# Kernel optimization log

Hardware: AMD Instinct MI355X
Metric: run time of the kernel (lower is better)

The kernel has to match this reference:

```python
import jax, jax.numpy as jnp
import numpy as np

NUM_GRAPHS = 16


def gat_layer(x, src, dst, n, W, a_s, a_d, b):
    # PyG GATConv, concat=False (mean over heads), negative_slope=0.2
    H, C = a_s.shape
    h = (x @ W).reshape(x.shape[0], H, C)            # [N,H,C]
    es = jnp.einsum('nhc,hc->nh', h, a_s)            # alpha_src per node
    ed = jnp.einsum('nhc,hc->nh', h, a_d)            # alpha_dst per node
    e = jax.nn.leaky_relu(es[src] + ed[dst], 0.2)    # [E,H]
    m = jax.ops.segment_max(e, dst, num_segments=n)
    m = jnp.where(jnp.isfinite(m), m, 0.0)
    p = jnp.exp(e - m[dst])
    denom = jax.ops.segment_sum(p, dst, num_segments=n)
    alpha = p / (denom[dst] + 1e-16)                 # segment softmax over in-edges
    out = jax.ops.segment_sum(h[src] * alpha[..., None], dst, num_segments=n)  # [N,H,C]
    return out.mean(axis=1) + b


def _forward(x, edge_index, batch,
             W_e0, a_s_e0, a_d_e0, b_e0, W_e1, a_s_e1, a_d_e1, b_e1,
             W_d0, a_s_d0, a_d_d0, b_d0, W_d1, a_s_d1, a_d_d1, b_d1,
             g_w1, g_b1, g_w2, g_b2):
    n = x.shape[0]
    loop = jnp.arange(n, dtype=edge_index.dtype)     # PyG add_self_loops=True
    src = jnp.concatenate([edge_index[0], loop])
    dst = jnp.concatenate([edge_index[1], loop])
    # encoder (dropout inert in eval)
    h = jax.nn.relu(gat_layer(x, src, dst, n, W_e0, a_s_e0, a_d_e0, b_e0))
    h = gat_layer(h, src, dst, n, W_e1, a_s_e1, a_d_e1, b_e1)
    # GlobalAttention pooling: gate MLP -> segment softmax over graphs -> scatter sum
    gate = (jax.nn.relu(h @ g_w1 + g_b1) @ g_w2 + g_b2)[:, 0]   # [N]
    gm = jax.ops.segment_max(gate, batch, num_segments=NUM_GRAPHS)
    gm = jnp.where(jnp.isfinite(gm), gm, 0.0)
    p = jnp.exp(gate - gm[batch])
    att = p / (jax.ops.segment_sum(p, batch, num_segments=NUM_GRAPHS)[batch] + 1e-16)
    pooled = jax.ops.segment_sum(att[:, None] * h, batch, num_segments=NUM_GRAPHS)
    h = pooled[batch]                                # broadcast pooled back to nodes
    # decoder (heads=1)
    h = jax.nn.relu(gat_layer(h, src, dst, n, W_d0, a_s_d0, a_d_d0, b_d0))
    return gat_layer(h, src, dst, n, W_d1, a_s_d1, a_d_d1, b_d1)


def setup_inputs() -> dict:
    key = jax.random.key(0)
    ks = jax.random.split(key, 24)
    N, E, Din, H, C = 50000, 250000, 128, 8, 64
    def w(k, shape, fan_in):
        return (jax.random.normal(k, shape, jnp.float32) / np.sqrt(fan_in)).astype(jnp.float32)
    return {
        'x': jax.random.normal(ks[0], (N, Din), jnp.float32),
        'edge_index': jax.random.randint(ks[1], (2, E), 0, N, dtype=jnp.int32),
        'batch': jnp.sort(jax.random.randint(ks[2], (N,), 0, NUM_GRAPHS, dtype=jnp.int32)),
        'W_e0': w(ks[3], (Din, H * C), Din), 'a_s_e0': w(ks[4], (H, C), C), 'a_d_e0': w(ks[5], (H, C), C), 'b_e0': w(ks[6], (C,), C),
        'W_e1': w(ks[7], (C, H * C), C), 'a_s_e1': w(ks[8], (H, C), C), 'a_d_e1': w(ks[9], (H, C), C), 'b_e1': w(ks[10], (C,), C),
        'W_d0': w(ks[11], (C, C), C), 'a_s_d0': w(ks[12], (1, C), C), 'a_d_d0': w(ks[13], (1, C), C), 'b_d0': w(ks[14], (C,), C),
        'W_d1': w(ks[15], (C, Din), C), 'a_s_d1': w(ks[16], (1, Din), Din), 'a_d_d1': w(ks[17], (1, Din), Din), 'b_d1': w(ks[18], (Din,), Din),
        'g_w1': w(ks[19], (C, C), C), 'g_b1': w(ks[20], (C,), C), 'g_w2': w(ks[21], (C, 1), C), 'g_b2': w(ks[22], (1,), C),
    }


def reference(x, edge_index, batch,
              W_e0, a_s_e0, a_d_e0, b_e0, W_e1, a_s_e1, a_d_e1, b_e1,
              W_d0, a_s_d0, a_d_d0, b_d0, W_d1, a_s_d1, a_d_d1, b_d1,
              g_w1, g_b1, g_w2, g_b2):
    return _forward(x, edge_index, batch,
                    W_e0, a_s_e0, a_d_e0, b_e0, W_e1, a_s_e1, a_d_e1, b_e1,
                    W_d0, a_s_d0, a_d_d0, b_d0, W_d1, a_s_d1, a_d_d1, b_d1,
                    g_w1, g_b1, g_w2, g_b2)
```

## Files before the change

kernel.cpp:

```cpp
#include <hip/hip_runtime.h>
#include <hip/hip_fp16.h>
#include <math.h>

#define TB 256

typedef _Float16 half8v __attribute__((ext_vector_type(8)));
typedef float float4v __attribute__((ext_vector_type(4)));

static __device__ __forceinline__ int edge_src(const int* ei, int E, int e) {
    return (e < E) ? ei[e] : (e - E);
}
static __device__ __forceinline__ int edge_dst(const int* ei, int E, int e) {
    return (e < E) ? ei[E + e] : (e - E);
}

__global__ void csr_count(const int* __restrict__ ei, int E, int Etot, int* __restrict__ cnt) {
    int e = blockIdx.x * blockDim.x + threadIdx.x;
    if (e >= Etot) return;
    atomicAdd(&cnt[edge_dst(ei, E, e)], 1);
}

__global__ __launch_bounds__(256) void scan_phase1(const int* __restrict__ cnt,
                                                   int* __restrict__ incl,
                                                   int* __restrict__ bsum, int n) {
    __shared__ int sdata[256];
    int t = threadIdx.x;
    int base = blockIdx.x * 256;
    int v = (base + t < n) ? cnt[base + t] : 0;
    for (int d = 1; d < 256; d <<= 1) {
        sdata[t] = v; __syncthreads();
        if (t >= d) v += sdata[t - d];
        __syncthreads();
    }
    if (base + t < n) incl[base + t] = v;
    if (t == 255) bsum[blockIdx.x] = v;
}

__global__ void scan_phase2(int* bsum, int nb) {
    __shared__ int sdata[256];
    int t = threadIdx.x;
    int v = (t < nb) ? bsum[t] : 0;
    for (int d = 1; d < 256; d <<= 1) {
        sdata[t] = v; __syncthreads();
        if (t >= d) v += sdata[t - d];
        __syncthreads();
    }
    if (t < nb) bsum[t] = v;
}

__global__ __launch_bounds__(256) void scan_phase3(const int* __restrict__ incl,
                                                   const int* __restrict__ bsum,
                                                   int* __restrict__ off, int n) {
    int i = blockIdx.x * 256 + threadIdx.x;
    if (i < n) off[i + 1] = incl[i] + (blockIdx.x ? bsum[blockIdx.x - 1] : 0);
    if (i == 0) off[0] = 0;
}

__global__ void csr_fill(const int* __restrict__ ei, int E, int Etot,
                         const int* __restrict__ off, int* __restrict__ cur,
                         int* __restrict__ esrc) {
    int e = blockIdx.x * blockDim.x + threadIdx.x;
    if (e >= Etot) return;
    int d = edge_dst(ei, E, e);
    int pos = atomicAdd(&cur[d], 1);
    esrc[off[d] + pos] = edge_src(ei, E, e);
}

__global__ void find_gstart(const int* __restrict__ batch, int* __restrict__ gstart, int N) {
    int n = blockIdx.x * blockDim.x + threadIdx.x;
    if (n >= N) return;
    int b = batch[n];
    int prev = n ? batch[n - 1] : -1;
    for (int g = prev + 1; g <= b; ++g) gstart[g] = n;
    if (n == N - 1)
        for (int g = b + 1; g <= 16; ++g) gstart[g] = N;
}

__global__ void cast_f2h(const float* __restrict__ in, __half* __restrict__ out, int n) {
    int i2 = (blockIdx.x * blockDim.x + threadIdx.x) * 2;
    if (i2 + 1 < n) {
        float2 v = *(const float2*)(in + i2);
        *(__half2*)(out + i2) = __floats2half2_rn(v.x, v.y);
    } else if (i2 < n) {
        out[i2] = __float2half(in[i2]);
    }
}

__global__ void make_ws(const float* __restrict__ W, const float* __restrict__ a_s,
                        const float* __restrict__ a_d, float* __restrict__ ws,
                        float* __restrict__ wd, int K, int H, int C) {
    int i = blockIdx.x * blockDim.x + threadIdx.x;
    if (i >= H * K) return;
    int h = i / K, k = i % K;
    const float* wrow = W + (size_t)k * H * C + h * C;
    float s = 0.f, d = 0.f;
    for (int c = 0; c < C; ++c) {
        s += wrow[c] * a_s[h * C + c];
        d += wrow[c] * a_d[h * C + c];
    }
    ws[i] = s;
    wd[i] = d;
}

__global__ void transpose_cast(const float* __restrict__ W, __half* __restrict__ WT,
                               int K, int N) {
    int i = blockIdx.x * blockDim.x + threadIdx.x;
    if (i >= N * K) return;
    int nn = i / K, kk = i % K;
    WT[i] = __float2half(W[kk * N + nn]);
}

__global__ void make_wstackT(const float* __restrict__ W, __half* __restrict__ WT,
                             int K, int H, int C) {
    int i = blockIdx.x * blockDim.x + threadIdx.x;
    if (i >= K * H * C) return;
    int c = i / (H * K);
    int rem = i % (H * K);
    int h = rem / K, k = rem % K;
    WT[i] = __float2half(W[(size_t)k * H * C + h * C + c]);
}

template <int K>
__global__ __launch_bounds__(256) void gemm_mfma(const __half* __restrict__ A,
                                                 const __half* __restrict__ BT,
                                                 __half* __restrict__ C,
                                                 int M, int N) {
    constexpr int KP = K + 8;
    __shared__ __align__(16) __half As[64 * KP];
    __shared__ __align__(16) __half Bs[64 * KP];
    int tid = threadIdx.x;
    int bm = blockIdx.y * 64, bn = blockIdx.x * 64;
    constexpr int LPR = K / 8;
    for (int idx = tid; idx < 64 * LPR; idx += 256) {
        int row = idx / LPR, koff = (idx % LPR) * 8;
        uint4 v = make_uint4(0u, 0u, 0u, 0u);
        int gr = bm + row;
        if (gr < M) v = *(const uint4*)(A + (size_t)gr * K + koff);
        *(uint4*)(&As[row * KP + koff]) = v;
        uint4 wv = *(const uint4*)(BT + (size_t)(bn + row) * K + koff);
        *(uint4*)(&Bs[row * KP + koff]) = wv;
    }
    __syncthreads();
    int wv_ = tid >> 6, l = tid & 63;
    int lr = l & 15, g = l >> 4;
    float4v acc[4] = {{0.f, 0.f, 0.f, 0.f}, {0.f, 0.f, 0.f, 0.f},
                      {0.f, 0.f, 0.f, 0.f}, {0.f, 0.f, 0.f, 0.f}};
    const __half* ap = &As[(16 * wv_ + lr) * KP + 8 * g];
    const __half* bp = &Bs[lr * KP + 8 * g];
#pragma unroll
    for (int k0 = 0; k0 < K; k0 += 32) {
        half8v af = *reinterpret_cast<const half8v*>(ap + k0);
#pragma unroll
        for (int nt = 0; nt < 4; ++nt) {
            half8v bf = *reinterpret_cast<const half8v*>(bp + nt * 16 * KP + k0);
            acc[nt] = __builtin_amdgcn_mfma_f32_16x16x32_f16(af, bf, acc[nt], 0, 0, 0);
        }
    }
#pragma unroll
    for (int nt = 0; nt < 4; ++nt) {
#pragma unroll
        for (int r = 0; r < 4; ++r) {
            int grow = bm + 16 * wv_ + 4 * g + r;
            if (grow < M)
                C[(size_t)grow * N + bn + nt * 16 + lr] = __float2half(acc[nt][r]);
        }
    }
}

template <int K, int H>
__global__ __launch_bounds__(256) void scores_nt(const __half* __restrict__ A,
                                                 const float* __restrict__ ws,
                                                 const float* __restrict__ wd,
                                                 float* __restrict__ es,
                                                 float* __restrict__ ed, int N) {
    int n = blockIdx.x * blockDim.x + threadIdx.x;
    if (n >= N) return;
    const __half* row = A + (size_t)n * K;
    float s[H] = {}, d[H] = {};
#pragma unroll
    for (int k0 = 0; k0 < K; k0 += 8) {
        uint4 raw = *(const uint4*)(row + k0);
        const __half* hv = (const __half*)&raw;
        float a[8];
#pragma unroll
        for (int q = 0; q < 8; ++q) a[q] = __half2float(hv[q]);
#pragma unroll
        for (int h = 0; h < H; ++h)
#pragma unroll
            for (int q = 0; q < 8; ++q) {
                s[h] += a[q] * ws[h * K + k0 + q];
                d[h] += a[q] * wd[h * K + k0 + q];
            }
    }
#pragma unroll
    for (int h = 0; h < H; ++h) {
        es[(size_t)n * H + h] = s[h];
        ed[(size_t)n * H + h] = d[h];
    }
}

template <bool RELU>
__global__ __launch_bounds__(256) void gat_gather_h8(const __half* __restrict__ hsrc,
                                                     const float* __restrict__ es,
                                                     const float* __restrict__ ed,
                                                     const int* __restrict__ off,
                                                     const int* __restrict__ esrc,
                                                     const float* __restrict__ bias,
                                                     __half* __restrict__ out, int N) {
    constexpr int HC = 512;
    int n = (blockIdx.x * blockDim.x + threadIdx.x) >> 6;
    int lane = threadIdx.x & 63;
    if (n >= N) return;
    int hd = lane >> 3;
    int k8 = lane >> 3, h8 = lane & 7;
    int j0 = off[n], j1 = off[n + 1];

    float edl = ed[(size_t)n * 8 + h8];

    float acc[8] = {};
    float denacc = 0.f;
    for (int j = j0; j < j1; j += 8) {
        int jj = j + k8;
        int jc = (jj < j1) ? jj : (j1 - 1);
        int sidx = esrc[jc];
        float v = es[(size_t)sidx * 8 + h8] + edl;
        v = (v > 0.f) ? v : 0.2f * v;
        float pm = (jj < j1) ? expf(v) : 0.f;
        denacc += pm;
        uint4 rw[8];
#pragma unroll
        for (int k = 0; k < 8; ++k) {
            int sb = __shfl(sidx, k * 8);
            rw[k] = *(const uint4*)(hsrc + (size_t)sb * HC + 8 * lane);
        }
#pragma unroll
        for (int k = 0; k < 8; ++k) {
            float a = __shfl(pm, k * 8 + hd);
            const __half* hv = (const __half*)&rw[k];
#pragma unroll
            for (int q = 0; q < 8; ++q) acc[q] += a * __half2float(hv[q]);
        }
    }

    float den = denacc;
#pragma unroll
    for (int o = 8; o < 64; o <<= 1) den += __shfl_xor(den, o);
    float dv = __shfl(den, hd) + 1e-16f;

#pragma unroll
    for (int q = 0; q < 8; ++q) acc[q] /= dv;
#pragma unroll
    for (int o = 8; o < 64; o <<= 1)
#pragma unroll
        for (int q = 0; q < 8; ++q) acc[q] += __shfl_xor(acc[q], o);

    if (lane < 8) {
        int cbase = 8 * lane;
        float r[8];
#pragma unroll
        for (int q = 0; q < 8; ++q) {
            float o2 = acc[q] * 0.125f + bias[cbase + q];
            if (RELU) o2 = fmaxf(o2, 0.f);
            r[q] = o2;
        }
        __half2 p0 = __floats2half2_rn(r[0], r[1]);
        __half2 p1 = __floats2half2_rn(r[2], r[3]);
        __half2 p2 = __floats2half2_rn(r[4], r[5]);
        __half2 p3 = __floats2half2_rn(r[6], r[7]);
        uint4 pk;
        pk.x = *(unsigned*)&p0; pk.y = *(unsigned*)&p1;
        pk.z = *(unsigned*)&p2; pk.w = *(unsigned*)&p3;
        *(uint4*)(out + (size_t)n * 64 + cbase) = pk;
    }
}

__global__ __launch_bounds__(256) void gat_gather_zh8(const __half* __restrict__ A,
                                                      const float* __restrict__ es,
                                                      const float* __restrict__ ed,
                                                      const int* __restrict__ off,
                                                      const int* __restrict__ esrc,
                                                      __half* __restrict__ z, int N) {
    int n = (blockIdx.x * blockDim.x + threadIdx.x) >> 6;
    int lane = threadIdx.x & 63;
    if (n >= N) return;
    int h = lane >> 3, q = lane & 7;
    int j0 = off[n], j1 = off[n + 1];
    float edv = ed[(size_t)n * 8 + h];

    float acc[8] = {};
    float den = 0.f;
    int j = j0;
    for (; j + 1 < j1; j += 2) {
        int s0 = esrc[j], s1 = esrc[j + 1];
        float v0 = es[(size_t)s0 * 8 + h] + edv;
        float v1 = es[(size_t)s1 * 8 + h] + edv;
        v0 = (v0 > 0.f) ? v0 : 0.2f * v0;
        v1 = (v1 > 0.f) ? v1 : 0.2f * v1;
        float p0 = expf(v0), p1 = expf(v1);
        den += p0 + p1;
        uint4 r0 = *(const uint4*)(A + (size_t)s0 * 64 + 8 * q);
        uint4 r1 = *(const uint4*)(A + (size_t)s1 * 64 + 8 * q);
        const __half* h0 = (const __half*)&r0;
        const __half* h1 = (const __half*)&r1;
#pragma unroll
        for (int k = 0; k < 8; ++k)
            acc[k] += p0 * __half2float(h0[k]) + p1 * __half2float(h1[k]);
    }
    if (j < j1) {
        int s0 = esrc[j];
        float v0 = es[(size_t)s0 * 8 + h] + edv;
        v0 = (v0 > 0.f) ? v0 : 0.2f * v0;
        float p0 = expf(v0);
        den += p0;
        uint4 r0 = *(const uint4*)(A + (size_t)s0 * 64 + 8 * q);
        const __half* h0 = (const __half*)&r0;
#pragma unroll
        for (int k = 0; k < 8; ++k) acc[k] += p0 * __half2float(h0[k]);
    }

    float inv = 1.f / ((den + 1e-16f) * 8.f);
    float r[8];
#pragma unroll
    for (int k = 0; k < 8; ++k) r[k] = acc[k] * inv;
    __half2 p0 = __floats2half2_rn(r[0], r[1]);
    __half2 p1 = __floats2half2_rn(r[2], r[3]);
    __half2 p2 = __floats2half2_rn(r[4], r[5]);
    __half2 p3 = __floats2half2_rn(r[6], r[7]);
    uint4 pk;
    pk.x = *(unsigned*)&p0; pk.y = *(unsigned*)&p1;
    pk.z = *(unsigned*)&p2; pk.w = *(unsigned*)&p3;
    *(uint4*)(z + (size_t)n * 512 + h * 64 + 8 * q) = pk;
}

__global__ __launch_bounds__(256) void gat_gather_z8(const __half* __restrict__ A,
                                                     const float* __restrict__ es,
                                                     const float* __restrict__ ed,
                                                     const int* __restrict__ off,
                                                     const int* __restrict__ esrc,
                                                     __half* __restrict__ z, int N) {
    int n = (blockIdx.x * blockDim.x + threadIdx.x) >> 6;
    int lane = threadIdx.x & 63;
    if (n >= N) return;
    int k8 = lane >> 3, q8 = lane & 7;
    int j0 = off[n], j1 = off[n + 1];
    float edv = ed[n];

    float acc[8] = {};
    float denacc = 0.f;
    for (int j = j0; j < j1; j += 8) {
        int jj = j + k8;
        int jc = (jj < j1) ? jj : (j1 - 1);
        int sidx = esrc[jc];
        float v = es[sidx] + edv;
        v = (v > 0.f) ? v : 0.2f * v;
        float pm = (jj < j1) ? expf(v) : 0.f;
        denacc += pm;
        uint4 rw = *(const uint4*)(A + (size_t)sidx * 64 + 8 * q8);
        const __half* hv = (const __half*)&rw;
#pragma unroll
        for (int q = 0; q < 8; ++q) acc[q] += pm * __half2float(hv[q]);
    }

    float den = denacc;
#pragma unroll
    for (int o = 8; o < 64; o <<= 1) {
        den += __shfl_xor(den, o);
#pragma unroll
        for (int q = 0; q < 8; ++q) acc[q] += __shfl_xor(acc[q], o);
    }
    float inv = 1.f / (den + 1e-16f);
    if (lane < 8) {
        float r[8];
#pragma unroll
        for (int q = 0; q < 8; ++q) r[q] = acc[q] * inv;
        __half2 p0 = __floats2half2_rn(r[0], r[1]);
        __half2 p1 = __floats2half2_rn(r[2], r[3]);
        __half2 p2 = __floats2half2_rn(r[4], r[5]);
        __half2 p3 = __floats2half2_rn(r[6], r[7]);
        uint4 pk;
        pk.x = *(unsigned*)&p0; pk.y = *(unsigned*)&p1;
        pk.z = *(unsigned*)&p2; pk.w = *(unsigned*)&p3;
        *(uint4*)(z + (size_t)n * 64 + 8 * lane) = pk;
    }
}

template <int KK, typename OUTT, bool RELU>
__global__ __launch_bounds__(256) void gemm_kt(const __half* __restrict__ A,
                                               const __half* __restrict__ BT,
                                               const float* __restrict__ bias,
                                               OUTT* __restrict__ C,
                                               int M, int Nout) {
    __shared__ __align__(16) __half As[64 * 72];
    __shared__ __align__(16) __half Bs[64 * 72];
    int tid = threadIdx.x;
    int bm = blockIdx.y * 64, bn = blockIdx.x * 64;
    int wv = tid >> 6, l = tid & 63, lr = l & 15, g = l >> 4;
    float4v acc[4] = {{0.f, 0.f, 0.f, 0.f}, {0.f, 0.f, 0.f, 0.f},
                      {0.f, 0.f, 0.f, 0.f}, {0.f, 0.f, 0.f, 0.f}};
    for (int kc = 0; kc < KK; kc += 64) {
        __syncthreads();
        for (int idx = tid; idx < 512; idx += 256) {
            int row = idx >> 3, ko = (idx & 7) * 8;
            uint4 v = make_uint4(0u, 0u, 0u, 0u);
            int gr = bm + row;
            if (gr < M) v = *(const uint4*)(A + (size_t)gr * KK + kc + ko);
            *(uint4*)(&As[row * 72 + ko]) = v;
            uint4 wvv = *(const uint4*)(BT + (size_t)(bn + row) * KK + kc + ko);
            *(uint4*)(&Bs[row * 72 + ko]) = wvv;
        }
        __syncthreads();
#pragma unroll
        for (int k0 = 0; k0 < 64; k0 += 32) {
            half8v af = *reinterpret_cast<const half8v*>(&As[(16 * wv + lr) * 72 + k0 + 8 * g]);
#pragma unroll
            for (int nt = 0; nt < 4; ++nt) {
                half8v bf = *reinterpret_cast<const half8v*>(&Bs[(nt * 16 + lr) * 72 + k0 + 8 * g]);
                acc[nt] = __builtin_amdgcn_mfma_f32_16x16x32_f16(af, bf, acc[nt], 0, 0, 0);
            }
        }
    }
#pragma unroll
    for (int nt = 0; nt < 4; ++nt) {
        float b = bias[bn + nt * 16 + lr];
#pragma unroll
        for (int r = 0; r < 4; ++r) {
            int grow = bm + 16 * wv + 4 * g + r;
            if (grow < M) {
                float c = acc[nt][r] + b;
                if (RELU) c = fmaxf(c, 0.f);
                if constexpr (sizeof(OUTT) == 2)
                    C[(size_t)grow * Nout + bn + nt * 16 + lr] = __float2half(c);
                else
                    C[(size_t)grow * Nout + bn + nt * 16 + lr] = c;
            }
        }
    }
}

__global__ __launch_bounds__(256) void gat_gather_d08(const float* __restrict__ hsrc,
                                                      const float* __restrict__ es16,
                                                      const float* __restrict__ ed16,
                                                      const int* __restrict__ off,
                                                      const int* __restrict__ esrc,
                                                      const int* __restrict__ batch,
                                                      const float* __restrict__ bias,
                                                      __half* __restrict__ out, int N) {
    int n = (blockIdx.x * blockDim.x + threadIdx.x) >> 6;
    int lane = threadIdx.x & 63;
    if (n >= N) return;
    int k8 = lane >> 3, q8 = lane & 7;
    int j0 = off[n], j1 = off[n + 1];
    float edv = ed16[batch[n]];

    float acc[8] = {};
    float denacc = 0.f;
    for (int j = j0; j < j1; j += 8) {
        int jj = j + k8;
        int jc = (jj < j1) ? jj : (j1 - 1);
        int g = batch[esrc[jc]];
        float v = es16[g] + edv;
        v = (v > 0.f) ? v : 0.2f * v;
        float pm = (jj < j1) ? expf(v) : 0.f;
        denacc += pm;
        const float* row = hsrc + (size_t)g * 64 + 8 * q8;
        float4 r0 = *(const float4*)row;
        float4 r1 = *(const float4*)(row + 4);
        acc[0] += pm * r0.x; acc[1] += pm * r0.y;
        acc[2] += pm * r0.z; acc[3] += pm * r0.w;
        acc[4] += pm * r1.x; acc[5] += pm * r1.y;
        acc[6] += pm * r1.z; acc[7] += pm * r1.w;
    }

    float den = denacc;
#pragma unroll
    for (int o = 8; o < 64; o <<= 1) {
        den += __shfl_xor(den, o);
#pragma unroll
        for (int q = 0; q < 8; ++q) acc[q] += __shfl_xor(acc[q], o);
    }
    float inv = 1.f / (den + 1e-16f);
    if (lane < 8) {
        float r[8];
#pragma unroll
        for (int q = 0; q < 8; ++q) r[q] = fmaxf(acc[q] * inv + bias[8 * lane + q], 0.f);
        __half2 p0 = __floats2half2_rn(r[0], r[1]);
        __half2 p1 = __floats2half2_rn(r[2], r[3]);
        __half2 p2 = __floats2half2_rn(r[4], r[5]);
        __half2 p3 = __floats2half2_rn(r[6], r[7]);
        uint4 pk;
        pk.x = *(unsigned*)&p0; pk.y = *(unsigned*)&p1;
        pk.z = *(unsigned*)&p2; pk.w = *(unsigned*)&p3;
        *(uint4*)(out + (size_t)n * 64 + 8 * lane) = pk;
    }
}

__global__ __launch_bounds__(256) void gate_mfma(const __half* __restrict__ A,
                                                 const __half* __restrict__ BT,
                                                 const float* __restrict__ b1,
                                                 const float* __restrict__ w2,
                                                 const float* __restrict__ b2,
                                                 const int* __restrict__ batch,
                                                 float* __restrict__ pg,
                                                 float* __restrict__ gden, int M) {
    constexpr int KP = 72;
    __shared__ __align__(16) __half As[64 * KP];
    __shared__ __align__(16) __half Bs[64 * KP];
    __shared__ float part[16];
    int tid = threadIdx.x;
    if (tid < 16) part[tid] = 0.f;
    int bm = blockIdx.x * 64;
    for (int idx = tid; idx < 512; idx += 256) {
        int row = idx >> 3, ko = (idx & 7) * 8;
        uint4 v = make_uint4(0u, 0u, 0u, 0u);
        int gr = bm + row;
        if (gr < M) v = *(const uint4*)(A + (size_t)gr * 64 + ko);
        *(uint4*)(&As[row * KP + ko]) = v;
        uint4 wvv = *(const uint4*)(BT + (size_t)row * 64 + ko);
        *(uint4*)(&Bs[row * KP + ko]) = wvv;
    }
    __syncthreads();
    int wv_ = tid >> 6, l = tid & 63;
    int lr = l & 15, g = l >> 4;
    float4v acc[4] = {{0.f, 0.f, 0.f, 0.f}, {0.f, 0.f, 0.f, 0.f},
                      {0.f, 0.f, 0.f, 0.f}, {0.f, 0.f, 0.f, 0.f}};
    const __half* ap = &As[(16 * wv_ + lr) * KP + 8 * g];
    const __half* bp = &Bs[lr * KP + 8 * g];
#pragma unroll
    for (int k0 = 0; k0 < 64; k0 += 32) {
        half8v af = *reinterpret_cast<const half8v*>(ap + k0);
#pragma unroll
        for (int nt = 0; nt < 4; ++nt) {
            half8v bf = *reinterpret_cast<const half8v*>(bp + nt * 16 * KP + k0);
            acc[nt] = __builtin_amdgcn_mfma_f32_16x16x32_f16(af, bf, acc[nt], 0, 0, 0);
        }
    }
    float partial[4];
#pragma unroll
    for (int r = 0; r < 4; ++r) {
        float t = 0.f;
#pragma unroll
        for (int nt = 0; nt < 4; ++nt) {
            int col = nt * 16 + lr;
            float tv = acc[nt][r] + b1[col];
            tv = fmaxf(tv, 0.f);
            t += tv * w2[col];
        }
        partial[r] = t;
    }
#pragma unroll
    for (int o = 1; o < 16; o <<= 1)
#pragma unroll
        for (int r = 0; r < 4; ++r) partial[r] += __shfl_xor(partial[r], o);
    if (lr == 0) {
        float bb = b2[0];
#pragma unroll
        for (int r = 0; r < 4; ++r) {
            int grow = bm + 16 * wv_ + 4 * g + r;
            if (grow < M) {
                float p = expf(partial[r] + bb);
                pg[grow] = p;
                atomicAdd(&part[batch[grow]], p);
            }
        }
    }
    __syncthreads();
    if (tid < 16 && part[tid] != 0.f) atomicAdd(&gden[tid], part[tid]);
}

#define POOL_SPLIT 32
__global__ __launch_bounds__(256) void pool_sum2(const __half* __restrict__ h,
                                                 const float* __restrict__ pg,
                                                 const int* __restrict__ gstart,
                                                 float* __restrict__ pooled, int N) {
    __shared__ float part[256];
    int g = blockIdx.x;
    int r0 = gstart[g], r1 = gstart[g + 1];
    int len = r1 - r0;
    int chunk = (len + POOL_SPLIT - 1) / POOL_SPLIT;
    int s0 = r0 + blockIdx.y * chunk;
    int s1 = min(s0 + chunk, r1);
    int wv = threadIdx.x >> 6, lane = threadIdx.x & 63;
    float acc = 0.f;
    for (int n = s0 + wv; n < s1; n += 4)
        acc += pg[n] * __half2float(h[(size_t)n * 64 + lane]);
    part[threadIdx.x] = acc;
    __syncthreads();
    if (threadIdx.x < 64) {
        float tot = part[threadIdx.x] + part[64 + threadIdx.x] +
                    part[128 + threadIdx.x] + part[192 + threadIdx.x];
        if (tot != 0.f) atomicAdd(&pooled[g * 64 + threadIdx.x], tot);
    }
}

__global__ void dec_prep(const float* __restrict__ pooled, const float* __restrict__ gden,
                         const float* __restrict__ Wd0, const float* __restrict__ asd,
                         const float* __restrict__ add, float* __restrict__ hd016,
                         float* __restrict__ es16, float* __restrict__ ed16) {
    int g = blockIdx.x;
    int lane = threadIdx.x;
    float pn = pooled[g * 64 + lane] / (gden[g] + 1e-16f);
    float o = 0.f;
    for (int c = 0; c < 64; ++c) o += __shfl(pn, c) * Wd0[c * 64 + lane];
    hd016[g * 64 + lane] = o;
    float s = o * asd[lane], d = o * add[lane];
#pragma unroll
    for (int off = 32; off; off >>= 1) {
        s += __shfl_xor(s, off);
        d += __shfl_xor(d, off);
    }
    if (lane == 0) {
        es16[g] = s;
        ed16[g] = d;
    }
}

static inline int cdiv(int a, int b) { return (a + b - 1) / b; }

extern "C" void kernel_launch(void* const* d_in, const int* in_sizes, int n_in,
                              void* d_out, int out_size, void* d_ws, size_t ws_size,
                              hipStream_t stream) {
    const float* x      = (const float*)d_in[0];
    const int*   ei     = (const int*)  d_in[1];
    const int*   batch  = (const int*)  d_in[2];
    const float* W_e0   = (const float*)d_in[3];
    const float* a_s_e0 = (const float*)d_in[4];
    const float* a_d_e0 = (const float*)d_in[5];
    const float* b_e0   = (const float*)d_in[6];
    const float* W_e1   = (const float*)d_in[7];
    const float* a_s_e1 = (const float*)d_in[8];
    const float* a_d_e1 = (const float*)d_in[9];
    const float* b_e1   = (const float*)d_in[10];
    const float* W_d0   = (const float*)d_in[11];
    const float* a_s_d0 = (const float*)d_in[12];
    const float* a_d_d0 = (const float*)d_in[13];
    const float* b_d0   = (const float*)d_in[14];
    const float* W_d1   = (const float*)d_in[15];
    const float* a_s_d1 = (const float*)d_in[16];
    const float* a_d_d1 = (const float*)d_in[17];
    const float* b_d1   = (const float*)d_in[18];
    const float* g_w1   = (const float*)d_in[19];
    const float* g_b1   = (const float*)d_in[20];
    const float* g_w2   = (const float*)d_in[21];
    const float* g_b2   = (const float*)d_in[22];

    const int N    = in_sizes[2];
    const int E    = in_sizes[1] / 2;
    const int Etot = E + N;
    const int Din  = in_sizes[0] / N;

    char* w = (char*)d_ws;
    size_t o = 0;
    auto alloc = [&](size_t bytes) -> void* {
        void* p = w + o;
        o = (o + bytes + 255) & ~(size_t)255;
        return p;
    };
    __half*   h16    = (__half*)  alloc((size_t)N * 512 * 2);
    __half*   x16    = (__half*)  alloc((size_t)N * Din * 2);
    __half*   bufA   = (__half*)  alloc((size_t)N * 64 * 2);
    __half*   bufB   = (__half*)  alloc((size_t)N * 64 * 2);
    __half*   wt_e0  = (__half*)  alloc((size_t)512 * 128 * 2);
    __half*   wst_e1 = (__half*)  alloc((size_t)64 * 512 * 2);
    __half*   wst_d1 = (__half*)  alloc((size_t)128 * 64 * 2);
    __half*   wt_g1  = (__half*)  alloc((size_t)64 * 64 * 2);
    float*    ws_e0  = (float*)   alloc(8 * 128 * 4);
    float*    wd_e0  = (float*)   alloc(8 * 128 * 4);
    float*    ws_e1  = (float*)   alloc(8 * 64 * 4);
    float*    wd_e1  = (float*)   alloc(8 * 64 * 4);
    float*    ws_d1  = (float*)   alloc(64 * 4);
    float*    wd_d1  = (float*)   alloc(64 * 4);
    float*    es     = (float*)   alloc((size_t)N * 8 * 4);
    float*    ed     = (float*)   alloc((size_t)N * 8 * 4);
    float*    pg     = (float*)   alloc((size_t)N * 4);
    int*      off    = (int*)     alloc((size_t)(N + 1) * 4);
    int*      cnt    = (int*)     alloc((size_t)N * 4);
    int*      esrc   = (int*)     alloc((size_t)Etot * 4);
    int*      bsum   = (int*)     alloc(256 * 4);
    int*      gstart = (int*)     alloc(17 * 4);
    float*    gden   = (float*)   alloc(16 * 4);
    float*    pooled = (float*)   alloc(16 * 64 * 4);
    float*    hd016  = (float*)   alloc(16 * 64 * 4);
    float*    es16   = (float*)   alloc(16 * 4);
    float*    ed16   = (float*)   alloc(16 * 4);
    (void)ws_size; (void)n_in; (void)out_size;

    const int nodeWaveGrid = cdiv(N, 4);
    const int nodeThreadGrid = cdiv(N, TB);
    const int edgeGrid     = cdiv(Etot, TB);
    const int scanBlocks   = cdiv(N, 256);

    hipMemsetAsync(cnt, 0, (size_t)N * 4, stream);
    csr_count<<<edgeGrid, TB, 0, stream>>>(ei, E, Etot, cnt);
    scan_phase1<<<scanBlocks, 256, 0, stream>>>(cnt, esrc , bsum, N);
    scan_phase2<<<1, 256, 0, stream>>>(bsum, scanBlocks);
    scan_phase3<<<scanBlocks, 256, 0, stream>>>(esrc, bsum, off, N);
    hipMemsetAsync(cnt, 0, (size_t)N * 4, stream);
    csr_fill<<<edgeGrid, TB, 0, stream>>>(ei, E, Etot, off, cnt, esrc);
    find_gstart<<<nodeThreadGrid, TB, 0, stream>>>(batch, gstart, N);

    cast_f2h<<<cdiv(N * Din / 2, TB), TB, 0, stream>>>(x, x16, N * Din);
    transpose_cast<<<cdiv(512 * 128, TB), TB, 0, stream>>>(W_e0, wt_e0, Din, 512);
    transpose_cast<<<cdiv(64 * 64, TB), TB, 0, stream>>>(g_w1, wt_g1, 64, 64);
    make_wstackT<<<cdiv(64 * 512, TB), TB, 0, stream>>>(W_e1, wst_e1, 64, 8, 64);
    make_wstackT<<<cdiv(128 * 64, TB), TB, 0, stream>>>(W_d1, wst_d1, 64, 1, 128);
    make_ws<<<cdiv(8 * 128, TB), TB, 0, stream>>>(W_e0, a_s_e0, a_d_e0, ws_e0, wd_e0, 128, 8, 64);
    make_ws<<<cdiv(8 * 64, TB), TB, 0, stream>>>(W_e1, a_s_e1, a_d_e1, ws_e1, wd_e1, 64, 8, 64);
    make_ws<<<1, TB, 0, stream>>>(W_d1, a_s_d1, a_d_d1, ws_d1, wd_d1, 64, 1, 128);

    scores_nt<128, 8><<<nodeThreadGrid, TB, 0, stream>>>(x16, ws_e0, wd_e0, es, ed, N);
    {
        dim3 grid(512 / 64, cdiv(N, 64));
        gemm_mfma<128><<<grid, TB, 0, stream>>>(x16, wt_e0, h16, N, 512);
    }
    gat_gather_h8<true><<<nodeWaveGrid, TB, 0, stream>>>(
        h16, es, ed, off, esrc, b_e0, bufA, N);

    scores_nt<64, 8><<<nodeThreadGrid, TB, 0, stream>>>(bufA, ws_e1, wd_e1, es, ed, N);
    gat_gather_zh8<<<nodeWaveGrid, TB, 0, stream>>>(bufA, es, ed, off, esrc, h16 , N);
    {
        dim3 grid(1, cdiv(N, 64));
        gemm_kt<512, __half, false><<<grid, TB, 0, stream>>>(h16 , wst_e1, b_e1, bufB, N, 64);
    }

    hipMemsetAsync(gden, 0, 16 * 4, stream);
    hipMemsetAsync(pooled, 0, 16 * 64 * 4, stream);
    gate_mfma<<<cdiv(N, 64), TB, 0, stream>>>(bufB, wt_g1, g_b1, g_w2, g_b2, batch, pg, gden, N);
    {
        dim3 grid(16, POOL_SPLIT);
        pool_sum2<<<grid, TB, 0, stream>>>(bufB, pg, gstart, pooled, N);
    }
    dec_prep<<<16, 64, 0, stream>>>(pooled, gden, W_d0, a_s_d0, a_d_d0, hd016, es16, ed16);

    gat_gather_d08<<<nodeWaveGrid, TB, 0, stream>>>(
        hd016, es16, ed16, off, esrc, batch, b_d0, bufA, N);

    scores_nt<64, 1><<<nodeThreadGrid, TB, 0, stream>>>(bufA, ws_d1, wd_d1, es, ed, N);
    gat_gather_z8<<<nodeWaveGrid, TB, 0, stream>>>(bufA, es, ed, off, esrc, h16 , N);
    {
        dim3 grid(2, cdiv(N, 64));
        gemm_kt<64, float, false><<<grid, TB, 0, stream>>>(h16 , wst_d1, b_d1, (float*)d_out, N, 128);
    }
}
```

Measured before the change: 352.6 us.

## Fuse weight prep kernels, fuse x cast into scores, widen first GEMM tile

The separate weight transpose/cast kernels and the three make_ws launches are merged into two launches. The fp32-to-fp16 cast of x is folded into the per-node score kernel, so x is read once instead of being cast and then reread. The first-layer GEMM now computes a 64x128 tile per block instead of 64x64, which halves how often A is reloaded but uses more LDS and accumulator registers per block. The combined score and cast kernel has each thread read a full fp32 row, which may coalesce poorly.

```diff
diff --git a/kernel.cpp b/kernel.cpp
--- a/kernel.cpp
+++ b/kernel.cpp
@@ -76,94 +76,142 @@
         for (int g = b + 1; g <= 16; ++g) gstart[g] = N;
 }
 
-__global__ void cast_f2h(const float* __restrict__ in, __half* __restrict__ out, int n) {
-    int i2 = (blockIdx.x * blockDim.x + threadIdx.x) * 2;
-    if (i2 + 1 < n) {
-        float2 v = *(const float2*)(in + i2);
-        *(__half2*)(out + i2) = __floats2half2_rn(v.x, v.y);
-    } else if (i2 < n) {
-        out[i2] = __float2half(in[i2]);
-    }
-}
-
-__global__ void make_ws(const float* __restrict__ W, const float* __restrict__ a_s,
-                        const float* __restrict__ a_d, float* __restrict__ ws,
-                        float* __restrict__ wd, int K, int H, int C) {
+__global__ void prep_weights(const float* __restrict__ W_e0, const float* __restrict__ g_w1,
+                             const float* __restrict__ W_e1, const float* __restrict__ W_d1,
+                             __half* __restrict__ wt_e0, __half* __restrict__ wt_g1,
+                             __half* __restrict__ wst_e1, __half* __restrict__ wst_d1) {
     int i = blockIdx.x * blockDim.x + threadIdx.x;
-    if (i >= H * K) return;
-    int h = i / K, k = i % K;
+    if (i < 65536) {
+        int nn = i / 128, kk = i % 128;
+        wt_e0[i] = __float2half(W_e0[kk * 512 + nn]);
+    } else if (i < 69632) {
+        int j = i - 65536;
+        int nn = j / 64, kk = j % 64;
+        wt_g1[j] = __float2half(g_w1[kk * 64 + nn]);
+    } else if (i < 102400) {
+        int j = i - 69632;
+        int c = j / 512, rem = j % 512;
+        int h = rem / 64, k = rem % 64;
+        wst_e1[j] = __float2half(W_e1[(size_t)k * 512 + h * 64 + c]);
+    } else if (i < 110592) {
+        int j = i - 102400;
+        int c = j / 64, k = j % 64;
+        wst_d1[j] = __float2half(W_d1[(size_t)k * 128 + c]);
+    }
+}
+
+__global__ void prep_ws(const float* __restrict__ W_e0, const float* __restrict__ a_s_e0,
+                        const float* __restrict__ a_d_e0,
+                        const float* __restrict__ W_e1, const float* __restrict__ a_s_e1,
+                        const float* __restrict__ a_d_e1,
+                        const float* __restrict__ W_d1, const float* __restrict__ a_s_d1,
+                        const float* __restrict__ a_d_d1,
+                        float* __restrict__ ws_e0, float* __restrict__ wd_e0,
+                        float* __restrict__ ws_e1, float* __restrict__ wd_e1,
+                        float* __restrict__ ws_d1, float* __restrict__ wd_d1) {
+    int i = blockIdx.x * blockDim.x + threadIdx.x;
+    const float* W; const float* as_; const float* ad_;
+    float* ws; float* wd;
+    int K, H, C, j;
+    if (i < 1024) { j = i; K = 128; H = 8; C = 64; W = W_e0; as_ = a_s_e0; ad_ = a_d_e0; ws = ws_e0; wd = wd_e0; }
+    else if (i < 1536) { j = i - 1024; K = 64; H = 8; C = 64; W = W_e1; as_ = a_s_e1; ad_ = a_d_e1; ws = ws_e1; wd = wd_e1; }
+    else if (i < 1600) { j = i - 1536; K = 64; H = 1; C = 128; W = W_d1; as_ = a_s_d1; ad_ = a_d_d1; ws = ws_d1; wd = wd_d1; }
+    else return;
+    int h = j / K, k = j % K;
     const float* wrow = W + (size_t)k * H * C + h * C;
     float s = 0.f, d = 0.f;
     for (int c = 0; c < C; ++c) {
-        s += wrow[c] * a_s[h * C + c];
-        d += wrow[c] * a_d[h * C + c];
-    }
-    ws[i] = s;
-    wd[i] = d;
-}
-
-__global__ void transpose_cast(const float* __restrict__ W, __half* __restrict__ WT,
-                               int K, int N) {
-    int i = blockIdx.x * blockDim.x + threadIdx.x;
-    if (i >= N * K) return;
-    int nn = i / K, kk = i % K;
-    WT[i] = __float2half(W[kk * N + nn]);
-}
-
-__global__ void make_wstackT(const float* __restrict__ W, __half* __restrict__ WT,
-                             int K, int H, int C) {
-    int i = blockIdx.x * blockDim.x + threadIdx.x;
-    if (i >= K * H * C) return;
-    int c = i / (H * K);
-    int rem = i % (H * K);
-    int h = rem / K, k = rem % K;
-    WT[i] = __float2half(W[(size_t)k * H * C + h * C + c]);
-}
-
-template <int K>
-__global__ __launch_bounds__(256) void gemm_mfma(const __half* __restrict__ A,
-                                                 const __half* __restrict__ BT,
-                                                 __half* __restrict__ C,
-                                                 int M, int N) {
-    constexpr int KP = K + 8;
+        s += wrow[c] * as_[h * C + c];
+        d += wrow[c] * ad_[h * C + c];
+    }
+    ws[j] = s;
+    wd[j] = d;
+}
+
+__global__ __launch_bounds__(256) void gemm_mfma_wide(const __half* __restrict__ A,
+                                                      const __half* __restrict__ BT,
+                                                      __half* __restrict__ C,
+                                                      int M, int N) {
+    constexpr int K = 128, KP = 136;
     __shared__ __align__(16) __half As[64 * KP];
-    __shared__ __align__(16) __half Bs[64 * KP];
+    __shared__ __align__(16) __half Bs[128 * KP];
     int tid = threadIdx.x;
-    int bm = blockIdx.y * 64, bn = blockIdx.x * 64;
-    constexpr int LPR = K / 8;
-    for (int idx = tid; idx < 64 * LPR; idx += 256) {
-        int row = idx / LPR, koff = (idx % LPR) * 8;
+    int bm = blockIdx.y * 64, bn = blockIdx.x * 128;
+    for (int idx = tid; idx < 64 * 16; idx += 256) {
+        int row = idx >> 4, ko = (idx & 15) * 8;
         uint4 v = make_uint4(0u, 0u, 0u, 0u);
         int gr = bm + row;
-        if (gr < M) v = *(const uint4*)(A + (size_t)gr * K + koff);
-        *(uint4*)(&As[row * KP + koff]) = v;
-        uint4 wv = *(const uint4*)(BT + (size_t)(bn + row) * K + koff);
-        *(uint4*)(&Bs[row * KP + koff]) = wv;
+        if (gr < M) v = *(const uint4*)(A + (size_t)gr * K + ko);
+        *(uint4*)(&As[row * KP + ko]) = v;
+    }
+    for (int idx = tid; idx < 128 * 16; idx += 256) {
+        int row = idx >> 4, ko = (idx & 15) * 8;
+        *(uint4*)(&Bs[row * KP + ko]) = *(const uint4*)(BT + (size_t)(bn + row) * K + ko);
     }
     __syncthreads();
     int wv_ = tid >> 6, l = tid & 63;
     int lr = l & 15, g = l >> 4;
-    float4v acc[4] = {{0.f, 0.f, 0.f, 0.f}, {0.f, 0.f, 0.f, 0.f},
-                      {0.f, 0.f, 0.f, 0.f}, {0.f, 0.f, 0.f, 0.f}};
+    float4v acc[8] = {{0,0,0,0},{0,0,0,0},{0,0,0,0},{0,0,0,0},
+                      {0,0,0,0},{0,0,0,0},{0,0,0,0},{0,0,0,0}};
     const __half* ap = &As[(16 * wv_ + lr) * KP + 8 * g];
     const __half* bp = &Bs[lr * KP + 8 * g];
 #pragma unroll
     for (int k0 = 0; k0 < K; k0 += 32) {
         half8v af = *reinterpret_cast<const half8v*>(ap + k0);
 #pragma unroll
-        for (int nt = 0; nt < 4; ++nt) {
+        for (int nt = 0; nt < 8; ++nt) {
             half8v bf = *reinterpret_cast<const half8v*>(bp + nt * 16 * KP + k0);
             acc[nt] = __builtin_amdgcn_mfma_f32_16x16x32_f16(af, bf, acc[nt], 0, 0, 0);
         }
     }
 #pragma unroll
-    for (int nt = 0; nt < 4; ++nt) {
+    for (int nt = 0; nt < 8; ++nt) {
 #pragma unroll
         for (int r = 0; r < 4; ++r) {
             int grow = bm + 16 * wv_ + 4 * g + r;
             if (grow < M)
                 C[(size_t)grow * N + bn + nt * 16 + lr] = __float2half(acc[nt][r]);
         }
+    }
+}
+
+template <int K, int H>
+__global__ __launch_bounds__(256) void scores_cast_nt(const float* __restrict__ X,
+                                                      __half* __restrict__ X16,
+                                                      const float* __restrict__ ws,
+                                                      const float* __restrict__ wd,
+                                                      float* __restrict__ es,
+                                                      float* __restrict__ ed, int N) {
+    int n = blockIdx.x * blockDim.x + threadIdx.x;
+    if (n >= N) return;
+    const float* row = X + (size_t)n * K;
+    __half* row16 = X16 + (size_t)n * K;
+    float s[H] = {}, d[H] = {};
+#pragma unroll
+    for (int k0 = 0; k0 < K; k0 += 8) {
+        float4 a0 = *(const float4*)(row + k0);
+        float4 a1 = *(const float4*)(row + k0 + 4);
+        float a[8] = {a0.x, a0.y, a0.z, a0.w, a1.x, a1.y, a1.z, a1.w};
+        __half2 h0 = __floats2half2_rn(a[0], a[1]);
+        __half2 h1 = __floats2half2_rn(a[2], a[3]);
+        __half2 h2 = __floats2half2_rn(a[4], a[5]);
+        __half2 h3 = __floats2half2_rn(a[6], a[7]);
+        uint4 pk;
+        pk.x = *(unsigned*)&h0; pk.y = *(unsigned*)&h1;
+        pk.z = *(unsigned*)&h2; pk.w = *(unsigned*)&h3;
+        *(uint4*)(row16 + k0) = pk;
+#pragma unroll
+        for (int h = 0; h < H; ++h)
+#pragma unroll
+            for (int q = 0; q < 8; ++q) {
+                s[h] += a[q] * ws[h * K + k0 + q];
+                d[h] += a[q] * wd[h * K + k0 + q];
+            }
+    }
+#pragma unroll
+    for (int h = 0; h < H; ++h) {
+        es[(size_t)n * H + h] = s[h];
+        ed[(size_t)n * H + h] = d[h];
     }
 }
 
@@ -698,19 +746,17 @@
     csr_fill<<<edgeGrid, TB, 0, stream>>>(ei, E, Etot, off, cnt, esrc);
     find_gstart<<<nodeThreadGrid, TB, 0, stream>>>(batch, gstart, N);
 
-    cast_f2h<<<cdiv(N * Din / 2, TB), TB, 0, stream>>>(x, x16, N * Din);
-    transpose_cast<<<cdiv(512 * 128, TB), TB, 0, stream>>>(W_e0, wt_e0, Din, 512);
-    transpose_cast<<<cdiv(64 * 64, TB), TB, 0, stream>>>(g_w1, wt_g1, 64, 64);
-    make_wstackT<<<cdiv(64 * 512, TB), TB, 0, stream>>>(W_e1, wst_e1, 64, 8, 64);
-    make_wstackT<<<cdiv(128 * 64, TB), TB, 0, stream>>>(W_d1, wst_d1, 64, 1, 128);
-    make_ws<<<cdiv(8 * 128, TB), TB, 0, stream>>>(W_e0, a_s_e0, a_d_e0, ws_e0, wd_e0, 128, 8, 64);
-    make_ws<<<cdiv(8 * 64, TB), TB, 0, stream>>>(W_e1, a_s_e1, a_d_e1, ws_e1, wd_e1, 64, 8, 64);
-    make_ws<<<1, TB, 0, stream>>>(W_d1, a_s_d1, a_d_d1, ws_d1, wd_d1, 64, 1, 128);
-
-    scores_nt<128, 8><<<nodeThreadGrid, TB, 0, stream>>>(x16, ws_e0, wd_e0, es, ed, N);
+    prep_weights<<<cdiv(110592, TB), TB, 0, stream>>>(W_e0, g_w1, W_e1, W_d1,
+                                                      wt_e0, wt_g1, wst_e1, wst_d1);
+    prep_ws<<<cdiv(1600, TB), TB, 0, stream>>>(W_e0, a_s_e0, a_d_e0,
+                                               W_e1, a_s_e1, a_d_e1,
+                                               W_d1, a_s_d1, a_d_d1,
+                                               ws_e0, wd_e0, ws_e1, wd_e1, ws_d1, wd_d1);
+
+    scores_cast_nt<128, 8><<<nodeThreadGrid, TB, 0, stream>>>(x, x16, ws_e0, wd_e0, es, ed, N);
     {
-        dim3 grid(512 / 64, cdiv(N, 64));
-        gemm_mfma<128><<<grid, TB, 0, stream>>>(x16, wt_e0, h16, N, 512);
+        dim3 grid(512 / 128, cdiv(N, 64));
+        gemm_mfma_wide<<<grid, TB, 0, stream>>>(x16, wt_e0, h16, N, 512);
     }
     gat_gather_h8<true><<<nodeWaveGrid, TB, 0, stream>>>(
         h16, es, ed, off, esrc, b_e0, bufA, N);
```

After: 338.3 us. -4.1%, faster.
